# Kernel tuning notes

Measured on AMD Instinct MI355X. Metric: run time of the kernel, lower is better.

The kernel has to match this reference:

```python
import jax, jax.numpy as jnp
import numpy as np

B, N, M, K, C = 2, 4096, 4096, 32, 64
RADIUS = 0.08


def _ball_query(d2, radius, k):
    # d2: (B, N, M) squared distances. Returns (B, N, k) int32 indices of the
    # first k in-radius neighbors (in index order); empty slots are filled with
    # the first found neighbor (or 0 if none), matching standard ball_query.
    m = d2.shape[-1]
    mask = d2 < radius * radius
    ar = jnp.arange(m, dtype=jnp.int32)
    key = jnp.where(mask, ar, ar + m)          # in-radius indices sort first
    neg_vals, _ = jax.lax.top_k(-key, k)       # k smallest keys
    vals = -neg_vals
    valid = vals < m
    raw = vals % m
    fill = raw[..., :1]                        # first neighbor (0 if none)
    return jnp.where(valid, raw, fill)


def setup_inputs() -> dict:
    key = jax.random.key(0)
    ks = jax.random.split(key, 9)
    points = jax.random.uniform(ks[0], (B, 3, N), dtype=jnp.float32)
    knnpoints = jax.random.uniform(ks[1], (B, 3, M), dtype=jnp.float32)
    feat = jax.random.normal(ks[2], (B, C, M), dtype=jnp.float32)
    w1 = jax.random.normal(ks[3], (128, C + 4), dtype=jnp.float32) * 0.05
    b1 = jnp.zeros((128,), jnp.float32)
    w2 = jax.random.normal(ks[4], (64, 128), dtype=jnp.float32) * 0.05
    b2 = jnp.zeros((64,), jnp.float32)
    w3 = jax.random.normal(ks[5], (64, 64), dtype=jnp.float32) * 0.05
    b3 = jnp.zeros((64,), jnp.float32)
    return {"points": points, "knnpoints": knnpoints, "feat": feat,
            "w1": w1, "b1": b1, "w2": w2, "b2": b2, "w3": w3, "b3": b3}


def reference(points, knnpoints, feat, w1, b1, w2, b2, w3, b3):
    # pairwise squared distances (B, N, M), computed once and reused by
    # ball_query and ChamferLoss
    pe = jnp.sum(points ** 2, axis=1)                       # (B, N)
    ke = jnp.sum(knnpoints ** 2, axis=1)                    # (B, M)
    cross = jnp.einsum('bdn,bdm->bnm', points, knnpoints)
    d2 = jnp.maximum(pe[:, :, None] + ke[:, None, :] - 2.0 * cross, 0.0)

    idx = _ball_query(jax.lax.stop_gradient(d2), RADIUS, K)  # (B, N, K)

    # gather neighbor coords / features: knnpoints[j, :, idx[j]]
    nb = jax.vmap(lambda p, i: p[:, i])(knnpoints, idx)      # (B, 3, N, K)
    nf = jax.vmap(lambda f, i: f[:, i])(feat, idx)           # (B, C, N, K)

    # relation features (neighbor_feature): diff + squared distance
    diff = nb - points[:, :, :, None]                        # (B, 3, N, K)
    dist = jnp.sum(diff ** 2, axis=1, keepdims=True)         # (B, 1, N, K)
    x = jnp.concatenate([nf, diff, dist], axis=1)            # (B, C+4, N, K)

    # SharedMLP: 1x1 conv stacks + ReLU
    h = jax.nn.relu(jnp.einsum('oc,bcnk->bonk', w1, x) + b1[None, :, None, None])
    h = jax.nn.relu(jnp.einsum('oc,bcnk->bonk', w2, h) + b2[None, :, None, None])
    h = jax.nn.relu(jnp.einsum('oc,bcnk->bonk', w3, h) + b3[None, :, None, None])
    agg = jnp.sum(h, axis=3)                                 # (B, 64, N)

    # ChamferLoss between points and knnpoints
    cd = jnp.sqrt(1e-6 + d2)
    loss = jnp.min(cd, axis=1).mean() + jnp.min(cd, axis=2).mean()
    return agg, loss
```

## Files before the change

### kernel.cpp

```cpp
#include <hip/hip_runtime.h>
#include <cstdint>

#define BB 2
#define NN 4096
#define MM 4096
#define KK 32
#define CC 64
#define R2C 0.0064f

typedef _Float16 v8h __attribute__((ext_vector_type(8)));
typedef _Float16 v4h __attribute__((ext_vector_type(4)));
typedef float    v4f __attribute__((ext_vector_type(4)));

__launch_bounds__(256)
__global__ void setup_kernel(const float* __restrict__ points,
                             const float* __restrict__ knn,
                             const float* __restrict__ feat,
                             const float* __restrict__ w1,
                             const float* __restrict__ w2,
                             const float* __restrict__ w3,
                             float4* __restrict__ pointsT,
                             float4* __restrict__ knnT,
                             _Float16* __restrict__ featH,
                             _Float16* __restrict__ w1h,
                             _Float16* __restrict__ w2h,
                             _Float16* __restrict__ w3h,
                             float* __restrict__ lossbuf) {
    __shared__ float tile[64][65];
    int blk = blockIdx.x, t = threadIdx.x;
    if (blk < 64) {
        const float* src = (blk < 32) ? points : knn;
        float4* dst = (blk < 32) ? pointsT : knnT;
        int i = (blk & 31) * 256 + t;
        int b = i >> 12, p = i & 4095;
        const float* base = src + (size_t)b * 3 * 4096;
        float x = base[p], y = base[4096 + p], z = base[8192 + p];
        float e = __fadd_rn(__fadd_rn(__fmul_rn(x, x), __fmul_rn(y, y)),
                            __fmul_rn(z, z));
        dst[i] = make_float4(x, y, z, e);
    } else if (blk < 192) {
        int tb = blk - 64;
        int b = tb / (MM / 64);
        int m0 = (tb % (MM / 64)) * 64;
        int mi = t & 63, cq = t >> 6;
        const float* src = feat + (size_t)b * CC * MM;
#pragma unroll
        for (int r = 0; r < 16; ++r) {
            int c = cq * 16 + r;
            tile[mi][c] = src[(size_t)c * MM + m0 + mi];
        }
        __syncthreads();
        int ci = t & 63, mq = t >> 6;
        _Float16* dst = featH + ((size_t)b * MM + m0) * CC;
#pragma unroll
        for (int r = 0; r < 16; ++r) {
            int mm = mq * 16 + r;
            dst[(size_t)mm * CC + ci] = (_Float16)tile[mm][ci];
        }
    } else if (blk < 240) {
        int tt = (blk - 192) * 256 + t;
        if (tt < 128 * 96) {
            int r = tt / 96, k = tt - r * 96;
            w1h[tt] = (_Float16)((k < 68) ? w1[r * 68 + k] : 0.0f);
        }
        if (tt < 64 * 128) w2h[tt] = (_Float16)w2[tt];
        if (tt < 64 * 64)  w3h[tt] = (_Float16)w3[tt];
    } else {
        int i = ((blk - 240) * 256 + t) * 4;
        *(float4*)(lossbuf + i) = make_float4(0.f, 0.f, 0.f, 0.f);
    }
}

__launch_bounds__(256)
__global__ void select_kernel(const float4* __restrict__ pointsT,
                              const float4* __restrict__ knnT,
                              int* __restrict__ idx_ws,
                              float* __restrict__ lossbuf) {
    __shared__ int sidx[4][KK];
    int t = threadIdx.x;
    int w = t >> 6, lane = t & 63;
    int pt = blockIdx.x * 4 + w;
    int b = pt >> 12;
    float4 p4 = pointsT[pt];
    const float4* kb = knnT + (size_t)b * MM;
    int cnt = 0;
    float minD = 1e30f;
    for (int c = 0; c < MM / 64; ++c) {
        int m = c * 64 + lane;
        float4 k4 = kb[m];
        float cross = __builtin_fmaf(p4.z, k4.z,
                      __builtin_fmaf(p4.y, k4.y, __fmul_rn(p4.x, k4.x)));
        float d2 = __fsub_rn(__fadd_rn(p4.w, k4.w), __fmul_rn(2.0f, cross));
        bool hit = d2 < R2C;
        minD = fminf(minD, fmaxf(d2, 0.0f));
        unsigned long long mask = __ballot(hit);
        if (hit) {
            int pos = cnt + __builtin_amdgcn_mbcnt_hi(
                              (unsigned)(mask >> 32),
                              __builtin_amdgcn_mbcnt_lo((unsigned)mask, 0));
            if (pos < KK) sidx[w][pos] = m;
        }
        cnt += __popcll(mask);
    }
    __syncthreads();
    if (lane < KK) {
        int fillv = (cnt > 0) ? sidx[w][0] : 0;
        int v = (lane < cnt) ? sidx[w][lane] : fillv;
        idx_ws[(size_t)pt * KK + lane] = v;
    }
    for (int off = 32; off > 0; off >>= 1)
        minD = fminf(minD, __shfl_xor(minD, off));
    if (lane == 0)
        atomicAdd(lossbuf + (pt & 1023) * 8,
                  sqrtf(1e-6f + minD) * (1.0f / (BB * NN)));
}

__launch_bounds__(256)
__global__ void colmin_kernel(const float4* __restrict__ pointsT,
                              const float4* __restrict__ knnT,
                              float* __restrict__ lossbuf) {
    int t = threadIdx.x;
    int w = t >> 6, lane = t & 63;
    int mp = blockIdx.x * 8 + w * 2;
    int b = mp >> 12;
    float4 kA = knnT[mp], kB = knnT[mp + 1];
    const float4* pb = pointsT + (size_t)b * NN;
    float minA = 1e30f, minB = 1e30f;
    for (int c = 0; c < NN / 64; ++c) {
        float4 p4 = pb[c * 64 + lane];
        float crA = __builtin_fmaf(p4.z, kA.z,
                    __builtin_fmaf(p4.y, kA.y, __fmul_rn(p4.x, kA.x)));
        float crB = __builtin_fmaf(p4.z, kB.z,
                    __builtin_fmaf(p4.y, kB.y, __fmul_rn(p4.x, kB.x)));
        float dA = __fsub_rn(__fadd_rn(p4.w, kA.w), __fmul_rn(2.0f, crA));
        float dB = __fsub_rn(__fadd_rn(p4.w, kB.w), __fmul_rn(2.0f, crB));
        minA = fminf(minA, fmaxf(dA, 0.0f));
        minB = fminf(minB, fmaxf(dB, 0.0f));
    }
    for (int off = 32; off > 0; off >>= 1) {
        minA = fminf(minA, __shfl_xor(minA, off));
        minB = fminf(minB, __shfl_xor(minB, off));
    }
    if (lane == 0)
        atomicAdd(lossbuf + ((mp >> 1) & 1023) * 8,
                  (sqrtf(1e-6f + minA) + sqrtf(1e-6f + minB)) * (1.0f / (BB * MM)));
}

#define TN  128
#define XS  104
#define H1S 136
#define H2S 72

__launch_bounds__(256, 2)
__global__ void mlp_kernel(const float4* __restrict__ pointsT,
                           const float4* __restrict__ knnT,
                           const _Float16* __restrict__ featH,
                           const int* __restrict__ idx_ws,
                           const _Float16* __restrict__ w1h, const float* __restrict__ b1,
                           const _Float16* __restrict__ w2h, const float* __restrict__ b2,
                           const _Float16* __restrict__ w3h, const float* __restrict__ b3,
                           const float* __restrict__ lossbuf,
                           float* __restrict__ out) {
    __shared__ __align__(16) _Float16 X[TN * XS];
    __shared__ __align__(16) _Float16 H1[TN * H1S];
    __shared__ __align__(16) _Float16 H2[TN * H2S];
    __shared__ float ws4[4];

    int t = threadIdx.x;

    if (blockIdx.x == 0) {
        float s = lossbuf[t * 8] + lossbuf[(t + 256) * 8] +
                  lossbuf[(t + 512) * 8] + lossbuf[(t + 768) * 8];
        for (int off = 32; off > 0; off >>= 1) s += __shfl_xor(s, off);
        if ((t & 63) == 0) ws4[t >> 6] = s;
        __syncthreads();
        if (t == 0)
            out[(size_t)BB * 64 * NN] = ws4[0] + ws4[1] + ws4[2] + ws4[3];
    }

    int point0 = blockIdx.x * 4;
    int b = point0 >> 12;
    int n0 = point0 & (NN - 1);

    {
        int col = t >> 1, half = t & 1;
        int pl = col >> 5, kk = col & 31;
        int n = n0 + pl;
        int id = idx_ws[(((size_t)b * NN + n) << 5) + kk];
        const v8h* src = (const v8h*)(featH + ((size_t)(b * MM + id)) * CC + half * 32);
        v8h f0 = src[0], f1 = src[1], f2 = src[2], f3 = src[3];
        v8h* dst = (v8h*)(X + col * XS + half * 32);
        dst[0] = f0; dst[1] = f1; dst[2] = f2; dst[3] = f3;
        if (half) {
            float4 p4 = pointsT[b * NN + n];
            float4 nb = knnT[b * MM + id];
            float dx = nb.x - p4.x, dy = nb.y - p4.y, dz = nb.z - p4.z;
            float dd = __fadd_rn(__fadd_rn(__fmul_rn(dx, dx), __fmul_rn(dy, dy)),
                                 __fmul_rn(dz, dz));
            v8h m0 = {(_Float16)dx, (_Float16)dy, (_Float16)dz, (_Float16)dd,
                      (_Float16)0.f, (_Float16)0.f, (_Float16)0.f, (_Float16)0.f};
            v8h z = {(_Float16)0.f, (_Float16)0.f, (_Float16)0.f, (_Float16)0.f,
                     (_Float16)0.f, (_Float16)0.f, (_Float16)0.f, (_Float16)0.f};
            v8h* md = (v8h*)(X + col * XS + 64);
            md[0] = m0; md[1] = z; md[2] = z; md[3] = z;
        }
    }

    int w = t >> 6, l = t & 63;
    int quad = l >> 4, lc = l & 15;

    v8h a1[2][3], a2[4], a3[2];
#pragma unroll
    for (int rt = 0; rt < 2; ++rt)
#pragma unroll
        for (int ks = 0; ks < 3; ++ks)
            a1[rt][ks] = *(const v8h*)(w1h + (32 * w + 16 * rt + lc) * 96 + 32 * ks + 8 * quad);
#pragma unroll
    for (int ks = 0; ks < 4; ++ks)
        a2[ks] = *(const v8h*)(w2h + (16 * w + lc) * 128 + 32 * ks + 8 * quad);
#pragma unroll
    for (int ks = 0; ks < 2; ++ks)
        a3[ks] = *(const v8h*)(w3h + (16 * w + lc) * 64 + 32 * ks + 8 * quad);

    v4f bias1a = *(const v4f*)(b1 + 32 * w + 4 * quad);
    v4f bias1b = *(const v4f*)(b1 + 32 * w + 16 + 4 * quad);
    v4f bias2  = *(const v4f*)(b2 + 16 * w + 4 * quad);
    v4f bias3  = *(const v4f*)(b3 + 16 * w + 4 * quad);

    __syncthreads();

#pragma unroll 1
    for (int ct = 0; ct < 8; ++ct) {
        int colb = 16 * ct + lc;
        v4f acc0 = bias1a, acc1 = bias1b;
#pragma unroll
        for (int ks = 0; ks < 3; ++ks) {
            v8h bx = *(const v8h*)(X + colb * XS + 32 * ks + 8 * quad);
            acc0 = __builtin_amdgcn_mfma_f32_16x16x32_f16(a1[0][ks], bx, acc0, 0, 0, 0);
            acc1 = __builtin_amdgcn_mfma_f32_16x16x32_f16(a1[1][ks], bx, acc1, 0, 0, 0);
        }
        v4h h0, h1v;
#pragma unroll
        for (int r = 0; r < 4; ++r) {
            h0[r]  = (_Float16)fmaxf(acc0[r], 0.0f);
            h1v[r] = (_Float16)fmaxf(acc1[r], 0.0f);
        }
        *(v4h*)(H1 + colb * H1S + 32 * w + 4 * quad)      = h0;
        *(v4h*)(H1 + colb * H1S + 32 * w + 16 + 4 * quad) = h1v;
    }
    __syncthreads();

#pragma unroll 1
    for (int ct = 0; ct < 8; ++ct) {
        int colb = 16 * ct + lc;
        v4f acc = bias2;
#pragma unroll
        for (int ks = 0; ks < 4; ++ks) {
            v8h bx = *(const v8h*)(H1 + colb * H1S + 32 * ks + 8 * quad);
            acc = __builtin_amdgcn_mfma_f32_16x16x32_f16(a2[ks], bx, acc, 0, 0, 0);
        }
        v4h h;
#pragma unroll
        for (int r = 0; r < 4; ++r) h[r] = (_Float16)fmaxf(acc[r], 0.0f);
        *(v4h*)(H2 + colb * H2S + 16 * w + 4 * quad) = h;
    }
    __syncthreads();

#pragma unroll 1
    for (int p = 0; p < 4; ++p) {
        int cA = (2 * p) * 16 + lc, cB = (2 * p + 1) * 16 + lc;
        v4f accA = bias3, accB = bias3;
#pragma unroll
        for (int ks = 0; ks < 2; ++ks) {
            v8h bA = *(const v8h*)(H2 + cA * H2S + 32 * ks + 8 * quad);
            v8h bB = *(const v8h*)(H2 + cB * H2S + 32 * ks + 8 * quad);
            accA = __builtin_amdgcn_mfma_f32_16x16x32_f16(a3[ks], bA, accA, 0, 0, 0);
            accB = __builtin_amdgcn_mfma_f32_16x16x32_f16(a3[ks], bB, accB, 0, 0, 0);
        }
        v4f s;
#pragma unroll
        for (int r = 0; r < 4; ++r)
            s[r] = fmaxf(accA[r], 0.0f) + fmaxf(accB[r], 0.0f);
#pragma unroll
        for (int off = 1; off < 16; off <<= 1) {
#pragma unroll
            for (int r = 0; r < 4; ++r) s[r] += __shfl_xor(s[r], off);
        }
        if (lc == 0) {
            int n = n0 + p;
            int rowb = 16 * w + 4 * quad;
#pragma unroll
            for (int r = 0; r < 4; ++r)
                out[((size_t)(b * 64 + rowb + r)) * NN + n] = s[r];
        }
    }
}

extern "C" void kernel_launch(void* const* d_in, const int* in_sizes, int n_in,
                              void* d_out, int out_size, void* d_ws, size_t ws_size,
                              hipStream_t stream) {
    const float* points = (const float*)d_in[0];
    const float* knn    = (const float*)d_in[1];
    const float* feat   = (const float*)d_in[2];
    const float* w1 = (const float*)d_in[3];
    const float* b1 = (const float*)d_in[4];
    const float* w2 = (const float*)d_in[5];
    const float* b2 = (const float*)d_in[6];
    const float* w3 = (const float*)d_in[7];
    const float* b3 = (const float*)d_in[8];
    float* out = (float*)d_out;

    char* ws = (char*)d_ws;
    float4*    pointsT = (float4*)ws;
    float4*    knnT    = (float4*)(ws + 131072);
    _Float16*  featH   = (_Float16*)(ws + 262144);
    int*       idx_ws  = (int*)(ws + 1310720);
    _Float16*  w1h     = (_Float16*)(ws + 2359296);
    _Float16*  w2h     = (_Float16*)(ws + 2383872);
    _Float16*  w3h     = (_Float16*)(ws + 2400256);
    float*     lossbuf = (float*)(ws + 2408448);

    setup_kernel<<<248, 256, 0, stream>>>(points, knn, feat, w1, w2, w3,
                                          pointsT, knnT, featH, w1h, w2h, w3h,
                                          lossbuf);
    select_kernel<<<(BB * NN) / 4, 256, 0, stream>>>(pointsT, knnT, idx_ws, lossbuf);
    colmin_kernel<<<(BB * MM) / 8, 256, 0, stream>>>(pointsT, knnT, lossbuf);
    mlp_kernel<<<(BB * NN) / 4, 256, 0, stream>>>(pointsT, knnT, featH, idx_ws,
                                                  w1h, b1, w2h, b2, w3h, b3,
                                                  lossbuf, out);
}
```

Measured before the change: 137.4 us.

## Merge select and colmin into tiled LDS scan; shrink MLP tile for occupancy

Replaces the separate ball-query select and column-min kernels with one scan kernel whose blocks stage 1024-point chunks of the candidate cloud in LDS. Each wave handles four query points, so every loaded point is reused four times and one launch is removed. The MLP kernel now processes 2 points (64 columns) per block, aliases H2 onto the X buffer and raises launch bounds to 4 blocks per CU for higher occupancy. The costs are more per-block overhead in the MLP, since weights are reloaded by twice as many blocks, and four ballots per inner iteration in the scan.

```diff
diff --git a/kernel.cpp b/kernel.cpp
--- a/kernel.cpp
+++ b/kernel.cpp
@@ -72,86 +72,125 @@
 }
 
 __launch_bounds__(256)
-__global__ void select_kernel(const float4* __restrict__ pointsT,
-                              const float4* __restrict__ knnT,
-                              int* __restrict__ idx_ws,
-                              float* __restrict__ lossbuf) {
-    __shared__ int sidx[4][KK];
+__global__ void scan_kernel(const float4* __restrict__ pointsT,
+                            const float4* __restrict__ knnT,
+                            int* __restrict__ idx_ws,
+                            float* __restrict__ lossbuf) {
+    __shared__ float4 tile[1024];
+    __shared__ int sidx[16][KK];
     int t = threadIdx.x;
     int w = t >> 6, lane = t & 63;
-    int pt = blockIdx.x * 4 + w;
-    int b = pt >> 12;
-    float4 p4 = pointsT[pt];
-    const float4* kb = knnT + (size_t)b * MM;
-    int cnt = 0;
-    float minD = 1e30f;
-    for (int c = 0; c < MM / 64; ++c) {
-        int m = c * 64 + lane;
-        float4 k4 = kb[m];
-        float cross = __builtin_fmaf(p4.z, k4.z,
-                      __builtin_fmaf(p4.y, k4.y, __fmul_rn(p4.x, k4.x)));
-        float d2 = __fsub_rn(__fadd_rn(p4.w, k4.w), __fmul_rn(2.0f, cross));
-        bool hit = d2 < R2C;
-        minD = fminf(minD, fmaxf(d2, 0.0f));
-        unsigned long long mask = __ballot(hit);
-        if (hit) {
-            int pos = cnt + __builtin_amdgcn_mbcnt_hi(
-                              (unsigned)(mask >> 32),
-                              __builtin_amdgcn_mbcnt_lo((unsigned)mask, 0));
-            if (pos < KK) sidx[w][pos] = m;
-        }
-        cnt += __popcll(mask);
-    }
-    __syncthreads();
-    if (lane < KK) {
-        int fillv = (cnt > 0) ? sidx[w][0] : 0;
-        int v = (lane < cnt) ? sidx[w][lane] : fillv;
-        idx_ws[(size_t)pt * KK + lane] = v;
-    }
-    for (int off = 32; off > 0; off >>= 1)
-        minD = fminf(minD, __shfl_xor(minD, off));
-    if (lane == 0)
-        atomicAdd(lossbuf + (pt & 1023) * 8,
-                  sqrtf(1e-6f + minD) * (1.0f / (BB * NN)));
+    int blk = blockIdx.x;
+
+    if (blk < 512) {
+        int pt0 = blk * 16;
+        int b = pt0 >> 12;
+        float4 P[4];
+#pragma unroll
+        for (int p = 0; p < 4; ++p) P[p] = pointsT[pt0 + 4 * w + p];
+        int cnt[4] = {0, 0, 0, 0};
+        float mn[4] = {1e30f, 1e30f, 1e30f, 1e30f};
+        const float4* kb = knnT + (size_t)b * MM;
+
+        for (int ch = 0; ch < 4; ++ch) {
+            const float4* src = kb + ch * 1024;
+            tile[t] = src[t]; tile[t + 256] = src[t + 256];
+            tile[t + 512] = src[t + 512]; tile[t + 768] = src[t + 768];
+            __syncthreads();
+#pragma unroll 2
+            for (int i = 0; i < 16; ++i) {
+                float4 k4 = tile[i * 64 + lane];
+                int m = ch * 1024 + i * 64 + lane;
+#pragma unroll
+                for (int p = 0; p < 4; ++p) {
+                    float cross = __builtin_fmaf(P[p].z, k4.z,
+                                  __builtin_fmaf(P[p].y, k4.y,
+                                                 __fmul_rn(P[p].x, k4.x)));
+                    float d2 = __fsub_rn(__fadd_rn(P[p].w, k4.w),
+                                         __fmul_rn(2.0f, cross));
+                    mn[p] = fminf(mn[p], fmaxf(d2, 0.0f));
+                    bool hit = d2 < R2C;
+                    unsigned long long mask = __ballot(hit);
+                    if (hit) {
+                        int pos = cnt[p] + __builtin_amdgcn_mbcnt_hi(
+                                     (unsigned)(mask >> 32),
+                                     __builtin_amdgcn_mbcnt_lo((unsigned)mask, 0));
+                        if (pos < KK) sidx[4 * w + p][pos] = m;
+                    }
+                    cnt[p] += __popcll(mask);
+                }
+            }
+            __syncthreads();
+        }
+
+        float lsum = 0.0f;
+#pragma unroll
+        for (int p = 0; p < 4; ++p) {
+            if (lane < KK) {
+                int row = 4 * w + p;
+                int fillv = (cnt[p] > 0) ? sidx[row][0] : 0;
+                int v = (lane < cnt[p]) ? sidx[row][lane] : fillv;
+                idx_ws[((size_t)(pt0 + row)) * KK + lane] = v;
+            }
+            float mv = mn[p];
+            for (int off = 32; off > 0; off >>= 1)
+                mv = fminf(mv, __shfl_xor(mv, off));
+            lsum += sqrtf(1e-6f + mv);
+        }
+        if (lane == 0)
+            atomicAdd(lossbuf + ((blk * 4 + w) & 1023) * 8,
+                      lsum * (1.0f / (BB * NN)));
+    } else {
+        int blk2 = blk - 512;
+        int m0 = blk2 * 16;
+        int b = m0 >> 12;
+        float4 Kp[4];
+#pragma unroll
+        for (int p = 0; p < 4; ++p) Kp[p] = knnT[m0 + 4 * w + p];
+        float mn[4] = {1e30f, 1e30f, 1e30f, 1e30f};
+        const float4* pb = pointsT + (size_t)b * NN;
+
+        for (int ch = 0; ch < 4; ++ch) {
+            const float4* src = pb + ch * 1024;
+            tile[t] = src[t]; tile[t + 256] = src[t + 256];
+            tile[t + 512] = src[t + 512]; tile[t + 768] = src[t + 768];
+            __syncthreads();
+#pragma unroll 2
+            for (int i = 0; i < 16; ++i) {
+                float4 p4 = tile[i * 64 + lane];
+#pragma unroll
+                for (int p = 0; p < 4; ++p) {
+                    float cross = __builtin_fmaf(p4.z, Kp[p].z,
+                                  __builtin_fmaf(p4.y, Kp[p].y,
+                                                 __fmul_rn(p4.x, Kp[p].x)));
+                    float d2 = __fsub_rn(__fadd_rn(p4.w, Kp[p].w),
+                                         __fmul_rn(2.0f, cross));
+                    mn[p] = fminf(mn[p], fmaxf(d2, 0.0f));
+                }
+            }
+            __syncthreads();
+        }
+
+        float lsum = 0.0f;
+#pragma unroll
+        for (int p = 0; p < 4; ++p) {
+            float mv = mn[p];
+            for (int off = 32; off > 0; off >>= 1)
+                mv = fminf(mv, __shfl_xor(mv, off));
+            lsum += sqrtf(1e-6f + mv);
+        }
+        if (lane == 0)
+            atomicAdd(lossbuf + ((blk2 * 4 + w) & 1023) * 8,
+                      lsum * (1.0f / (BB * MM)));
+    }
 }
 
-__launch_bounds__(256)
-__global__ void colmin_kernel(const float4* __restrict__ pointsT,
-                              const float4* __restrict__ knnT,
-                              float* __restrict__ lossbuf) {
-    int t = threadIdx.x;
-    int w = t >> 6, lane = t & 63;
-    int mp = blockIdx.x * 8 + w * 2;
-    int b = mp >> 12;
-    float4 kA = knnT[mp], kB = knnT[mp + 1];
-    const float4* pb = pointsT + (size_t)b * NN;
-    float minA = 1e30f, minB = 1e30f;
-    for (int c = 0; c < NN / 64; ++c) {
-        float4 p4 = pb[c * 64 + lane];
-        float crA = __builtin_fmaf(p4.z, kA.z,
-                    __builtin_fmaf(p4.y, kA.y, __fmul_rn(p4.x, kA.x)));
-        float crB = __builtin_fmaf(p4.z, kB.z,
-                    __builtin_fmaf(p4.y, kB.y, __fmul_rn(p4.x, kB.x)));
-        float dA = __fsub_rn(__fadd_rn(p4.w, kA.w), __fmul_rn(2.0f, crA));
-        float dB = __fsub_rn(__fadd_rn(p4.w, kB.w), __fmul_rn(2.0f, crB));
-        minA = fminf(minA, fmaxf(dA, 0.0f));
-        minB = fminf(minB, fmaxf(dB, 0.0f));
-    }
-    for (int off = 32; off > 0; off >>= 1) {
-        minA = fminf(minA, __shfl_xor(minA, off));
-        minB = fminf(minB, __shfl_xor(minB, off));
-    }
-    if (lane == 0)
-        atomicAdd(lossbuf + ((mp >> 1) & 1023) * 8,
-                  (sqrtf(1e-6f + minA) + sqrtf(1e-6f + minB)) * (1.0f / (BB * MM)));
-}
-
-#define TN  128
+#define TC  64
 #define XS  104
 #define H1S 136
 #define H2S 72
 
-__launch_bounds__(256, 2)
+__launch_bounds__(256, 4)
 __global__ void mlp_kernel(const float4* __restrict__ pointsT,
                            const float4* __restrict__ knnT,
                            const _Float16* __restrict__ featH,
@@ -161,9 +200,10 @@
                            const _Float16* __restrict__ w3h, const float* __restrict__ b3,
                            const float* __restrict__ lossbuf,
                            float* __restrict__ out) {
-    __shared__ __align__(16) _Float16 X[TN * XS];
-    __shared__ __align__(16) _Float16 H1[TN * H1S];
-    __shared__ __align__(16) _Float16 H2[TN * H2S];
+    __shared__ __align__(16) _Float16 SM[TC * XS + TC * H1S];
+    _Float16* X  = SM;
+    _Float16* H2 = SM;
+    _Float16* H1 = SM + TC * XS;
     __shared__ float ws4[4];
 
     int t = threadIdx.x;
@@ -178,32 +218,31 @@
             out[(size_t)BB * 64 * NN] = ws4[0] + ws4[1] + ws4[2] + ws4[3];
     }
 
-    int point0 = blockIdx.x * 4;
+    int point0 = blockIdx.x * 2;
     int b = point0 >> 12;
     int n0 = point0 & (NN - 1);
 
     {
-        int col = t >> 1, half = t & 1;
+        int col = t >> 2, h = t & 3;
         int pl = col >> 5, kk = col & 31;
         int n = n0 + pl;
         int id = idx_ws[(((size_t)b * NN + n) << 5) + kk];
-        const v8h* src = (const v8h*)(featH + ((size_t)(b * MM + id)) * CC + half * 32);
-        v8h f0 = src[0], f1 = src[1], f2 = src[2], f3 = src[3];
-        v8h* dst = (v8h*)(X + col * XS + half * 32);
-        dst[0] = f0; dst[1] = f1; dst[2] = f2; dst[3] = f3;
-        if (half) {
+        const v8h* src = (const v8h*)(featH + ((size_t)(b * MM + id)) * CC) + h * 2;
+        v8h f0 = src[0], f1 = src[1];
+        v8h* dst = (v8h*)(X + col * XS) + h * 2;
+        dst[0] = f0; dst[1] = f1;
+        v8h mv = {(_Float16)0.f, (_Float16)0.f, (_Float16)0.f, (_Float16)0.f,
+                  (_Float16)0.f, (_Float16)0.f, (_Float16)0.f, (_Float16)0.f};
+        if (h == 0) {
             float4 p4 = pointsT[b * NN + n];
             float4 nb = knnT[b * MM + id];
             float dx = nb.x - p4.x, dy = nb.y - p4.y, dz = nb.z - p4.z;
             float dd = __fadd_rn(__fadd_rn(__fmul_rn(dx, dx), __fmul_rn(dy, dy)),
                                  __fmul_rn(dz, dz));
-            v8h m0 = {(_Float16)dx, (_Float16)dy, (_Float16)dz, (_Float16)dd,
-                      (_Float16)0.f, (_Float16)0.f, (_Float16)0.f, (_Float16)0.f};
-            v8h z = {(_Float16)0.f, (_Float16)0.f, (_Float16)0.f, (_Float16)0.f,
-                     (_Float16)0.f, (_Float16)0.f, (_Float16)0.f, (_Float16)0.f};
-            v8h* md = (v8h*)(X + col * XS + 64);
-            md[0] = m0; md[1] = z; md[2] = z; md[3] = z;
-        }
+            mv[0] = (_Float16)dx; mv[1] = (_Float16)dy;
+            mv[2] = (_Float16)dz; mv[3] = (_Float16)dd;
+        }
+        *((v8h*)(X + col * XS + 64) + h) = mv;
     }
 
     int w = t >> 6, l = t & 63;
@@ -230,7 +269,7 @@
     __syncthreads();
 
 #pragma unroll 1
-    for (int ct = 0; ct < 8; ++ct) {
+    for (int ct = 0; ct < 4; ++ct) {
         int colb = 16 * ct + lc;
         v4f acc0 = bias1a, acc1 = bias1b;
 #pragma unroll
@@ -251,7 +290,7 @@
     __syncthreads();
 
 #pragma unroll 1
-    for (int ct = 0; ct < 8; ++ct) {
+    for (int ct = 0; ct < 4; ++ct) {
         int colb = 16 * ct + lc;
         v4f acc = bias2;
 #pragma unroll
@@ -267,7 +306,7 @@
     __syncthreads();
 
 #pragma unroll 1
-    for (int p = 0; p < 4; ++p) {
+    for (int p = 0; p < 2; ++p) {
         int cA = (2 * p) * 16 + lc, cB = (2 * p + 1) * 16 + lc;
         v4f accA = bias3, accB = bias3;
 #pragma unroll
@@ -323,9 +362,8 @@
     setup_kernel<<<248, 256, 0, stream>>>(points, knn, feat, w1, w2, w3,
                                           pointsT, knnT, featH, w1h, w2h, w3h,
                                           lossbuf);
-    select_kernel<<<(BB * NN) / 4, 256, 0, stream>>>(pointsT, knnT, idx_ws, lossbuf);
-    colmin_kernel<<<(BB * MM) / 8, 256, 0, stream>>>(pointsT, knnT, lossbuf);
-    mlp_kernel<<<(BB * NN) / 4, 256, 0, stream>>>(pointsT, knnT, featH, idx_ws,
+    scan_kernel<<<1024, 256, 0, stream>>>(pointsT, knnT, idx_ws, lossbuf);
+    mlp_kernel<<<(BB * NN) / 2, 256, 0, stream>>>(pointsT, knnT, featH, idx_ws,
                                                   w1h, b1, w2h, b2, w3h, b3,
                                                   lossbuf, out);
 }
```

Result: faster. 121.4 us (-11.7%).
